# Kernel tuning notes

Measured on AMD Instinct MI355X. Metric: run time of the kernel, lower is better.

## Reference

```python
import jax, jax.numpy as jnp
import numpy as np

S_Q = 2048; B = 2; H = 16; D = 128
SCALE = 1.0 / np.sqrt(128.0)  # softmax_scale from init


def setup_inputs() -> dict:
    key = jax.random.key(0)
    kq, kk, kv, ks = jax.random.split(key, 4)
    q = jax.random.normal(kq, (S_Q, B, H, D), dtype=jnp.float32)
    k = jax.random.normal(kk, (S_Q, B, 1, D), dtype=jnp.float32)   # MQA: H_kv=1
    v = jax.random.normal(kv, (S_Q, B, 1, D), dtype=jnp.float32)
    sinks = jax.random.normal(ks, (H,), dtype=jnp.float32)         # learned per-head sink logits
    return {"q": q, "k": k, "v": v, "sinks": sinks, "mask": 0}


def reference(q, k, v, sinks, mask):
    # q: [S_q, B, H, D]; k, v: [S_k, B, H_kv, D] (H_kv may be 1 -> MQA expand)
    S_q, Bn, Hq, Dn = q.shape
    S_k = k.shape[0]
    k = jnp.broadcast_to(k, (S_k, Bn, Hq, Dn))
    v = jnp.broadcast_to(v, (S_k, Bn, Hq, Dn))
    # logits: [B, H, S_q, S_k]
    logits = jnp.einsum("sbhd,tbhd->bhst", q.astype(jnp.float32), k.astype(jnp.float32)) * SCALE
    # causal mask (triu(-inf, diag=1) added in original)
    causal = jnp.tril(jnp.ones((S_q, S_k), dtype=bool))
    logits = jnp.where(causal[None, None], logits, -jnp.inf)
    # sink-augmented softmax: append sink logit as extra column, softmax, drop it
    sink = sinks.astype(jnp.float32)[None, :, None, None]        # [1, H, 1, 1]
    m = jax.lax.stop_gradient(jnp.maximum(logits.max(axis=-1, keepdims=True), sink))
    e = jnp.exp(logits - m)                                      # [B, H, S_q, S_k]
    denom = e.sum(axis=-1, keepdims=True) + jnp.exp(sink - m)    # sink column contribution
    probs = e / denom
    out = jnp.einsum("bhst,tbhd->sbhd", probs.astype(v.dtype), v)  # [S_q, B, H, D]
    return out.reshape(S_q, Bn, Hq * Dn)
```

## Files before the change

kernel.cpp:

```cpp
#include <hip/hip_runtime.h>

#define SQ 2048
#define NB 2
#define NH 16
#define DH 128
#define NT32 64
#define NQT 32
#define SCALE_L2E 0.1275174609f
#define LOG2E 1.4426950408889634f
#define DEFER_THR 11.0f

typedef _Float16 f16x8 __attribute__((ext_vector_type(8)));
typedef _Float16 f16x4 __attribute__((ext_vector_type(4)));
typedef float f32x4 __attribute__((ext_vector_type(4)));

static __device__ __forceinline__ _Float16 f2h(float f) { return (_Float16)f; }

__global__ __launch_bounds__(256)
void prepack(const float* __restrict__ k, const float* __restrict__ v,
             _Float16* __restrict__ kws, _Float16* __restrict__ vws) {
    const int bid   = blockIdx.x;
    const int which = bid >> 7;
    const int b     = (bid >> 6) & 1;
    const int t     = bid & 63;
    const int tid   = threadIdx.x;

    if (which == 0) {
        const float* kbase = k + (size_t)t * 32 * (NB * DH) + b * DH;
        _Float16* dst = kws + ((size_t)b * NT32 + t) * 4096;
        #pragma unroll
        for (int p = 0; p < 4; ++p) {
            const int id4 = p * 256 + tid;
            const int row = id4 >> 5;
            const int c0  = (id4 & 31) << 2;
            f32x4 a = *(const f32x4*)(kbase + (size_t)row * (NB * DH) + c0);
            const int e = (row * 128 + c0) ^ ((row & 7) << 3);
            f16x4 pk = { f2h(a.x), f2h(a.y), f2h(a.z), f2h(a.w) };
            *(f16x4*)(dst + e) = pk;
        }
    } else {
        const float* vbase = v + b * DH;
        _Float16* dst = vws + ((size_t)b * NT32 + t) * 4096;
        const int d    = tid & 127;
        const int half = tid >> 7;
        #pragma unroll
        for (int p = 0; p < 4; ++p) {
            const int c0 = (p * 2 + half) * 4;
            float a0 = vbase[(size_t)(t * 32 + c0 + 0) * (NB * DH) + d];
            float a1 = vbase[(size_t)(t * 32 + c0 + 1) * (NB * DH) + d];
            float a2 = vbase[(size_t)(t * 32 + c0 + 2) * (NB * DH) + d];
            float a3 = vbase[(size_t)(t * 32 + c0 + 3) * (NB * DH) + d];
            const int e = (d * 32 + c0) ^ ((d & 7) << 3);
            f16x4 pk = { f2h(a0), f2h(a1), f2h(a2), f2h(a3) };
            *(f16x4*)(dst + e) = pk;
        }
    }
}

static __device__ __forceinline__ void gload16(const _Float16* gsrc, _Float16* ldst) {
    __builtin_amdgcn_global_load_lds(
        (const __attribute__((address_space(1))) void*)gsrc,
        (__attribute__((address_space(3))) void*)ldst, 16, 0, 0);
}

__global__ __launch_bounds__(256, 4)
void attn_fwd(const float* __restrict__ q, const _Float16* __restrict__ kws,
              const _Float16* __restrict__ vws, const float* __restrict__ sinks,
              float* __restrict__ out) {
    __shared__ _Float16 Kb[2][4096];
    __shared__ _Float16 Vb[2][4096];
    __shared__ _Float16 Plds[4][512];

    const int tid  = threadIdx.x;
    const int w    = tid >> 6;
    const int lane = tid & 63;
    const int r    = lane & 15;
    const int g    = lane >> 4;

    const int bid   = blockIdx.x;
    const int bh    = bid & 31;
    const int b     = bh & 1;
    const int h     = bh >> 1;
    const int qtIdx = bid >> 5;
    const int jj    = qtIdx & 7;
    const int mm    = qtIdx >> 3;
    const int qt = (mm == 0) ? jj : (mm == 1) ? 15 - jj
                 : (mm == 2) ? 16 + jj : 31 - jj;
    const int q0 = qt * 64;
    const int sq = q0 + w * 16 + r;

    f16x8 qf[4];
    {
        const float* qrow = q + ((size_t)sq * NB + b) * (NH * DH) + h * DH;
        #pragma unroll
        for (int kc = 0; kc < 4; ++kc) {
            const int d0 = kc * 32 + g * 8;
            f32x4 a = *(const f32x4*)(qrow + d0);
            f32x4 c = *(const f32x4*)(qrow + d0 + 4);
            f16x8 t;
            t[0] = f2h(a.x * SCALE_L2E); t[1] = f2h(a.y * SCALE_L2E);
            t[2] = f2h(a.z * SCALE_L2E); t[3] = f2h(a.w * SCALE_L2E);
            t[4] = f2h(c.x * SCALE_L2E); t[5] = f2h(c.y * SCALE_L2E);
            t[6] = f2h(c.z * SCALE_L2E); t[7] = f2h(c.w * SCALE_L2E);
            qf[kc] = t;
        }
    }

    float m_run = sinks[h] * LOG2E;
    float l_run = 1.0f;
    f32x4 acc[8];
    #pragma unroll
    for (int i = 0; i < 8; ++i) acc[i] = (f32x4)(0.0f);

    const _Float16* ktiles = kws + (size_t)b * NT32 * 4096;
    const _Float16* vtiles = vws + (size_t)b * NT32 * 4096;
    const int ntiles = 2 * qt + 2;
    const int wlimit = q0 + w * 16 + 15;

    #pragma unroll
    for (int p = 0; p < 2; ++p) {
        const int off = (p * 256 + tid) * 8;
        gload16(ktiles + off, &Kb[0][off]);
        gload16(vtiles + off, &Vb[0][off]);
    }
    asm volatile("s_waitcnt vmcnt(0)" ::: "memory");
    __builtin_amdgcn_s_barrier();

    for (int it = 0; it < ntiles; ++it) {
        const int cur = it & 1;
        if (it + 1 < ntiles) {
            const _Float16* kn = ktiles + (size_t)(it + 1) * 4096;
            const _Float16* vn = vtiles + (size_t)(it + 1) * 4096;
            #pragma unroll
            for (int p = 0; p < 2; ++p) {
                const int off = (p * 256 + tid) * 8;
                gload16(kn + off, &Kb[cur ^ 1][off]);
                gload16(vn + off, &Vb[cur ^ 1][off]);
            }
        }

        const int ktb = it * 32;
        if (ktb <= wlimit) {
            float sv[8];
            #pragma unroll
            for (int ct = 0; ct < 2; ++ct) {
                f32x4 sa = (f32x4)(0.0f);
                const int c = ct * 16 + r;
                #pragma unroll
                for (int kc = 0; kc < 4; ++kc) {
                    const int e = (c * 128 + kc * 32 + g * 8) ^ ((c & 7) << 3);
                    f16x8 kf = *(const f16x8*)(&Kb[cur][e]);
                    sa = __builtin_amdgcn_mfma_f32_16x16x32_f16(kf, qf[kc], sa, 0, 0, 0);
                }
                #pragma unroll
                for (int i = 0; i < 4; ++i) sv[ct * 4 + i] = sa[i];
            }

            if (ktb + 31 > q0 + w * 16) {
                #pragma unroll
                for (int ct = 0; ct < 2; ++ct)
                    #pragma unroll
                    for (int i = 0; i < 4; ++i) {
                        const int tk = ktb + ct * 16 + g * 4 + i;
                        if (tk > sq) sv[ct * 4 + i] = -1e30f;
                    }
            }

            float a0 = fmaxf(sv[0], sv[1]), a1 = fmaxf(sv[2], sv[3]);
            float a2 = fmaxf(sv[4], sv[5]), a3 = fmaxf(sv[6], sv[7]);
            float mx = fmaxf(fmaxf(a0, a1), fmaxf(a2, a3));
            mx = fmaxf(mx, __shfl_xor(mx, 16));
            mx = fmaxf(mx, __shfl_xor(mx, 32));

            if (!__all(mx <= m_run + DEFER_THR)) {
                const float mnew = fmaxf(m_run, mx);
                const float corr = __builtin_amdgcn_exp2f(m_run - mnew);
                m_run = mnew;
                l_run *= corr;
                #pragma unroll
                for (int i = 0; i < 4; ++i) {
                    const float ci = __shfl(corr, (lane & 48) | (g * 4 + i));
                    #pragma unroll
                    for (int nb = 0; nb < 8; ++nb) acc[nb][i] *= ci;
                }
            }

            #pragma unroll
            for (int i = 0; i < 8; ++i)
                sv[i] = __builtin_amdgcn_exp2f(sv[i] - m_run);
            float s0 = (sv[0] + sv[1]) + (sv[2] + sv[3]);
            float s1 = (sv[4] + sv[5]) + (sv[6] + sv[7]);
            float ls = s0 + s1;
            ls += __shfl_xor(ls, 16);
            ls += __shfl_xor(ls, 32);
            l_run += ls;

            #pragma unroll
            for (int ct = 0; ct < 2; ++ct) {
                f16x4 pb = { f2h(sv[ct * 4 + 0]), f2h(sv[ct * 4 + 1]),
                             f2h(sv[ct * 4 + 2]), f2h(sv[ct * 4 + 3]) };
                const int c0 = ct * 16 + g * 4;
                const int e = (r * 32 + c0) ^ ((r & 7) << 3);
                *(f16x4*)(&Plds[w][e]) = pb;
            }

            const int ep = (r * 32 + g * 8) ^ ((r & 7) << 3);
            f16x8 pf = *(const f16x8*)(&Plds[w][ep]);
            #pragma unroll
            for (int nb = 0; nb < 8; ++nb) {
                const int d = nb * 16 + r;
                const int ev = (d * 32 + g * 8) ^ ((d & 7) << 3);
                f16x8 vf = *(const f16x8*)(&Vb[cur][ev]);
                acc[nb] = __builtin_amdgcn_mfma_f32_16x16x32_f16(pf, vf, acc[nb], 0, 0, 0);
            }
        }

        asm volatile("s_waitcnt vmcnt(0)" ::: "memory");
        __builtin_amdgcn_s_barrier();
    }

    #pragma unroll
    for (int i = 0; i < 4; ++i) {
        const float li = __shfl(l_run, (lane & 48) | (g * 4 + i));
        const float rl = 1.0f / li;
        const int row = q0 + w * 16 + g * 4 + i;
        float* op = out + ((size_t)row * NB + b) * (NH * DH) + h * DH + r;
        #pragma unroll
        for (int nb = 0; nb < 8; ++nb)
            op[nb * 16] = acc[nb][i] * rl;
    }
}

extern "C" void kernel_launch(void* const* d_in, const int* in_sizes, int n_in,
                              void* d_out, int out_size, void* d_ws, size_t ws_size,
                              hipStream_t stream) {
    const float* q     = (const float*)d_in[0];
    const float* k     = (const float*)d_in[1];
    const float* v     = (const float*)d_in[2];
    const float* sinks = (const float*)d_in[3];
    float* out = (float*)d_out;

    _Float16* kws = (_Float16*)d_ws;
    _Float16* vws = kws + (size_t)NB * NT32 * 4096;

    prepack<<<dim3(256), 256, 0, stream>>>(k, v, kws, vws);
    attn_fwd<<<dim3(NQT * NB * NH), 256, 0, stream>>>(q, kws, vws, sinks, out);
}
```

Before: 89.60 us.

## Pair low/high causal query tiles per block and widen KV tiles to 64

```diff
diff --git a/kernel.cpp b/kernel.cpp
--- a/kernel.cpp
+++ b/kernel.cpp
@@ -4,7 +4,7 @@
 #define NB 2
 #define NH 16
 #define DH 128
-#define NT32 64
+#define NKT 32
 #define NQT 32
 #define SCALE_L2E 0.1275174609f
 #define LOG2E 1.4426950408889634f
@@ -20,16 +20,16 @@
 void prepack(const float* __restrict__ k, const float* __restrict__ v,
              _Float16* __restrict__ kws, _Float16* __restrict__ vws) {
     const int bid   = blockIdx.x;
-    const int which = bid >> 7;
-    const int b     = (bid >> 6) & 1;
-    const int t     = bid & 63;
+    const int which = bid >> 6;
+    const int b     = (bid >> 5) & 1;
+    const int t     = bid & 31;
     const int tid   = threadIdx.x;
 
     if (which == 0) {
-        const float* kbase = k + (size_t)t * 32 * (NB * DH) + b * DH;
-        _Float16* dst = kws + ((size_t)b * NT32 + t) * 4096;
-        #pragma unroll
-        for (int p = 0; p < 4; ++p) {
+        const float* kbase = k + (size_t)t * 64 * (NB * DH) + b * DH;
+        _Float16* dst = kws + ((size_t)b * NKT + t) * 8192;
+        #pragma unroll
+        for (int p = 0; p < 8; ++p) {
             const int id4 = p * 256 + tid;
             const int row = id4 >> 5;
             const int c0  = (id4 & 31) << 2;
@@ -40,17 +40,17 @@
         }
     } else {
         const float* vbase = v + b * DH;
-        _Float16* dst = vws + ((size_t)b * NT32 + t) * 4096;
+        _Float16* dst = vws + ((size_t)b * NKT + t) * 8192;
         const int d    = tid & 127;
         const int half = tid >> 7;
         #pragma unroll
-        for (int p = 0; p < 4; ++p) {
+        for (int p = 0; p < 8; ++p) {
             const int c0 = (p * 2 + half) * 4;
-            float a0 = vbase[(size_t)(t * 32 + c0 + 0) * (NB * DH) + d];
-            float a1 = vbase[(size_t)(t * 32 + c0 + 1) * (NB * DH) + d];
-            float a2 = vbase[(size_t)(t * 32 + c0 + 2) * (NB * DH) + d];
-            float a3 = vbase[(size_t)(t * 32 + c0 + 3) * (NB * DH) + d];
-            const int e = (d * 32 + c0) ^ ((d & 7) << 3);
+            float a0 = vbase[(size_t)(t * 64 + c0 + 0) * (NB * DH) + d];
+            float a1 = vbase[(size_t)(t * 64 + c0 + 1) * (NB * DH) + d];
+            float a2 = vbase[(size_t)(t * 64 + c0 + 2) * (NB * DH) + d];
+            float a3 = vbase[(size_t)(t * 64 + c0 + 3) * (NB * DH) + d];
+            const int e = (d * 64 + c0) ^ ((d & 7) << 3);
             f16x4 pk = { f2h(a0), f2h(a1), f2h(a2), f2h(a3) };
             *(f16x4*)(dst + e) = pk;
         }
@@ -63,13 +63,100 @@
         (__attribute__((address_space(3))) void*)ldst, 16, 0, 0);
 }
 
-__global__ __launch_bounds__(256, 4)
+static __device__ __forceinline__ void tile_update(
+    const _Float16* __restrict__ Kc, const _Float16* __restrict__ Vc,
+    _Float16* __restrict__ Pw, const f16x8* __restrict__ qf,
+    f32x4* __restrict__ acc, float& m_run, float& l_run,
+    int ktb, int sq, int q0w, int r, int g, int lane) {
+
+    float sv[16];
+    #pragma unroll
+    for (int ct = 0; ct < 4; ++ct) {
+        f32x4 sa = (f32x4)(0.0f);
+        const int c = ct * 16 + r;
+        #pragma unroll
+        for (int kc = 0; kc < 4; ++kc) {
+            const int e = (c * 128 + kc * 32 + g * 8) ^ ((c & 7) << 3);
+            f16x8 kf = *(const f16x8*)(&Kc[e]);
+            sa = __builtin_amdgcn_mfma_f32_16x16x32_f16(kf, qf[kc], sa, 0, 0, 0);
+        }
+        #pragma unroll
+        for (int i = 0; i < 4; ++i) sv[ct * 4 + i] = sa[i];
+    }
+
+    if (ktb + 63 > q0w) {
+        #pragma unroll
+        for (int ct = 0; ct < 4; ++ct)
+            #pragma unroll
+            for (int i = 0; i < 4; ++i) {
+                const int tk = ktb + ct * 16 + g * 4 + i;
+                if (tk > sq) sv[ct * 4 + i] = -1e30f;
+            }
+    }
+
+    float m0 = fmaxf(fmaxf(sv[0], sv[1]), fmaxf(sv[2], sv[3]));
+    float m1 = fmaxf(fmaxf(sv[4], sv[5]), fmaxf(sv[6], sv[7]));
+    float m2 = fmaxf(fmaxf(sv[8], sv[9]), fmaxf(sv[10], sv[11]));
+    float m3 = fmaxf(fmaxf(sv[12], sv[13]), fmaxf(sv[14], sv[15]));
+    float mx = fmaxf(fmaxf(m0, m1), fmaxf(m2, m3));
+    mx = fmaxf(mx, __shfl_xor(mx, 16));
+    mx = fmaxf(mx, __shfl_xor(mx, 32));
+
+    if (!__all(mx <= m_run + DEFER_THR)) {
+        const float mnew = fmaxf(m_run, mx);
+        const float corr = __builtin_amdgcn_exp2f(m_run - mnew);
+        m_run = mnew;
+        l_run *= corr;
+        #pragma unroll
+        for (int i = 0; i < 4; ++i) {
+            const float ci = __shfl(corr, (lane & 48) | (g * 4 + i));
+            #pragma unroll
+            for (int nb = 0; nb < 8; ++nb) acc[nb][i] *= ci;
+        }
+    }
+
+    #pragma unroll
+    for (int i = 0; i < 16; ++i)
+        sv[i] = __builtin_amdgcn_exp2f(sv[i] - m_run);
+    float t0 = (sv[0] + sv[1]) + (sv[2] + sv[3]);
+    float t1 = (sv[4] + sv[5]) + (sv[6] + sv[7]);
+    float t2 = (sv[8] + sv[9]) + (sv[10] + sv[11]);
+    float t3 = (sv[12] + sv[13]) + (sv[14] + sv[15]);
+    float ls = (t0 + t1) + (t2 + t3);
+    ls += __shfl_xor(ls, 16);
+    ls += __shfl_xor(ls, 32);
+    l_run += ls;
+
+    #pragma unroll
+    for (int ct = 0; ct < 4; ++ct) {
+        f16x4 pb = { f2h(sv[ct * 4 + 0]), f2h(sv[ct * 4 + 1]),
+                     f2h(sv[ct * 4 + 2]), f2h(sv[ct * 4 + 3]) };
+        const int c0 = ct * 16 + g * 4;
+        const int e = (r * 64 + c0) ^ ((r & 7) << 3);
+        *(f16x4*)(&Pw[e]) = pb;
+    }
+
+    #pragma unroll
+    for (int cc = 0; cc < 2; ++cc) {
+        const int ep = (r * 64 + cc * 32 + g * 8) ^ ((r & 7) << 3);
+        f16x8 pf = *(const f16x8*)(&Pw[ep]);
+        #pragma unroll
+        for (int nb = 0; nb < 8; ++nb) {
+            const int d = nb * 16 + r;
+            const int ev = (d * 64 + cc * 32 + g * 8) ^ ((d & 7) << 3);
+            f16x8 vf = *(const f16x8*)(&Vc[ev]);
+            acc[nb] = __builtin_amdgcn_mfma_f32_16x16x32_f16(pf, vf, acc[nb], 0, 0, 0);
+        }
+    }
+}
+
+__global__ __launch_bounds__(256, 2)
 void attn_fwd(const float* __restrict__ q, const _Float16* __restrict__ kws,
               const _Float16* __restrict__ vws, const float* __restrict__ sinks,
               float* __restrict__ out) {
-    __shared__ _Float16 Kb[2][4096];
-    __shared__ _Float16 Vb[2][4096];
-    __shared__ _Float16 Plds[4][512];
+    __shared__ _Float16 Kb[2][8192];
+    __shared__ _Float16 Vb[2][8192];
+    __shared__ _Float16 Plds[4][1024];
 
     const int tid  = threadIdx.x;
     const int w    = tid >> 6;
@@ -77,20 +164,20 @@
     const int r    = lane & 15;
     const int g    = lane >> 4;
 
-    const int bid   = blockIdx.x;
-    const int bh    = bid & 31;
-    const int b     = bh & 1;
-    const int h     = bh >> 1;
-    const int qtIdx = bid >> 5;
-    const int jj    = qtIdx & 7;
-    const int mm    = qtIdx >> 3;
-    const int qt = (mm == 0) ? jj : (mm == 1) ? 15 - jj
-                 : (mm == 2) ? 16 + jj : 31 - jj;
-    const int q0 = qt * 64;
-    const int sq = q0 + w * 16 + r;
-
-    f16x8 qf[4];
-    {
+    const int bid = blockIdx.x;
+    const int bh  = bid & 31;
+    const int b   = bh & 1;
+    const int h   = bh >> 1;
+    const int j   = bid >> 5;
+    const int qtL = j, qtH = NQT - 1 - j;
+    const int q0L = qtL * 64, q0H = qtH * 64;
+    const int sqL = q0L + w * 16 + r, sqH = q0H + w * 16 + r;
+
+    f16x8 qfL[4], qfH[4];
+    #pragma unroll
+    for (int ctx = 0; ctx < 2; ++ctx) {
+        const int sq = ctx ? sqH : sqL;
+        f16x8* qf = ctx ? qfH : qfL;
         const float* qrow = q + ((size_t)sq * NB + b) * (NH * DH) + h * DH;
         #pragma unroll
         for (int kc = 0; kc < 4; ++kc) {
@@ -106,19 +193,18 @@
         }
     }
 
-    float m_run = sinks[h] * LOG2E;
-    float l_run = 1.0f;
-    f32x4 acc[8];
-    #pragma unroll
-    for (int i = 0; i < 8; ++i) acc[i] = (f32x4)(0.0f);
-
-    const _Float16* ktiles = kws + (size_t)b * NT32 * 4096;
-    const _Float16* vtiles = vws + (size_t)b * NT32 * 4096;
-    const int ntiles = 2 * qt + 2;
-    const int wlimit = q0 + w * 16 + 15;
-
-    #pragma unroll
-    for (int p = 0; p < 2; ++p) {
+    const float sink2 = sinks[h] * LOG2E;
+    float mL = sink2, lL = 1.0f, mH = sink2, lH = 1.0f;
+    f32x4 accL[8], accH[8];
+    #pragma unroll
+    for (int i = 0; i < 8; ++i) { accL[i] = (f32x4)(0.0f); accH[i] = (f32x4)(0.0f); }
+
+    const _Float16* ktiles = kws + (size_t)b * NKT * 8192;
+    const _Float16* vtiles = vws + (size_t)b * NKT * 8192;
+    const int ntiles = qtH + 1;
+
+    #pragma unroll
+    for (int p = 0; p < 4; ++p) {
         const int off = (p * 256 + tid) * 8;
         gload16(ktiles + off, &Kb[0][off]);
         gload16(vtiles + off, &Vb[0][off]);
@@ -129,105 +215,43 @@
     for (int it = 0; it < ntiles; ++it) {
         const int cur = it & 1;
         if (it + 1 < ntiles) {
-            const _Float16* kn = ktiles + (size_t)(it + 1) * 4096;
-            const _Float16* vn = vtiles + (size_t)(it + 1) * 4096;
-            #pragma unroll
-            for (int p = 0; p < 2; ++p) {
+            const _Float16* kn = ktiles + (size_t)(it + 1) * 8192;
+            const _Float16* vn = vtiles + (size_t)(it + 1) * 8192;
+            #pragma unroll
+            for (int p = 0; p < 4; ++p) {
                 const int off = (p * 256 + tid) * 8;
                 gload16(kn + off, &Kb[cur ^ 1][off]);
                 gload16(vn + off, &Vb[cur ^ 1][off]);
             }
         }
 
-        const int ktb = it * 32;
-        if (ktb <= wlimit) {
-            float sv[8];
-            #pragma unroll
-            for (int ct = 0; ct < 2; ++ct) {
-                f32x4 sa = (f32x4)(0.0f);
-                const int c = ct * 16 + r;
-                #pragma unroll
-                for (int kc = 0; kc < 4; ++kc) {
-                    const int e = (c * 128 + kc * 32 + g * 8) ^ ((c & 7) << 3);
-                    f16x8 kf = *(const f16x8*)(&Kb[cur][e]);
-                    sa = __builtin_amdgcn_mfma_f32_16x16x32_f16(kf, qf[kc], sa, 0, 0, 0);
-                }
-                #pragma unroll
-                for (int i = 0; i < 4; ++i) sv[ct * 4 + i] = sa[i];
-            }
-
-            if (ktb + 31 > q0 + w * 16) {
-                #pragma unroll
-                for (int ct = 0; ct < 2; ++ct)
-                    #pragma unroll
-                    for (int i = 0; i < 4; ++i) {
-                        const int tk = ktb + ct * 16 + g * 4 + i;
-                        if (tk > sq) sv[ct * 4 + i] = -1e30f;
-                    }
-            }
-
-            float a0 = fmaxf(sv[0], sv[1]), a1 = fmaxf(sv[2], sv[3]);
-            float a2 = fmaxf(sv[4], sv[5]), a3 = fmaxf(sv[6], sv[7]);
-            float mx = fmaxf(fmaxf(a0, a1), fmaxf(a2, a3));
-            mx = fmaxf(mx, __shfl_xor(mx, 16));
-            mx = fmaxf(mx, __shfl_xor(mx, 32));
-
-            if (!__all(mx <= m_run + DEFER_THR)) {
-                const float mnew = fmaxf(m_run, mx);
-                const float corr = __builtin_amdgcn_exp2f(m_run - mnew);
-                m_run = mnew;
-                l_run *= corr;
-                #pragma unroll
-                for (int i = 0; i < 4; ++i) {
-                    const float ci = __shfl(corr, (lane & 48) | (g * 4 + i));
-                    #pragma unroll
-                    for (int nb = 0; nb < 8; ++nb) acc[nb][i] *= ci;
-                }
-            }
-
-            #pragma unroll
-            for (int i = 0; i < 8; ++i)
-                sv[i] = __builtin_amdgcn_exp2f(sv[i] - m_run);
-            float s0 = (sv[0] + sv[1]) + (sv[2] + sv[3]);
-            float s1 = (sv[4] + sv[5]) + (sv[6] + sv[7]);
-            float ls = s0 + s1;
-            ls += __shfl_xor(ls, 16);
-            ls += __shfl_xor(ls, 32);
-            l_run += ls;
-
-            #pragma unroll
-            for (int ct = 0; ct < 2; ++ct) {
-                f16x4 pb = { f2h(sv[ct * 4 + 0]), f2h(sv[ct * 4 + 1]),
-                             f2h(sv[ct * 4 + 2]), f2h(sv[ct * 4 + 3]) };
-                const int c0 = ct * 16 + g * 4;
-                const int e = (r * 32 + c0) ^ ((r & 7) << 3);
-                *(f16x4*)(&Plds[w][e]) = pb;
-            }
-
-            const int ep = (r * 32 + g * 8) ^ ((r & 7) << 3);
-            f16x8 pf = *(const f16x8*)(&Plds[w][ep]);
-            #pragma unroll
-            for (int nb = 0; nb < 8; ++nb) {
-                const int d = nb * 16 + r;
-                const int ev = (d * 32 + g * 8) ^ ((d & 7) << 3);
-                f16x8 vf = *(const f16x8*)(&Vb[cur][ev]);
-                acc[nb] = __builtin_amdgcn_mfma_f32_16x16x32_f16(pf, vf, acc[nb], 0, 0, 0);
-            }
-        }
+        const int ktb = it * 64;
+        if (ktb <= q0H + w * 16 + 15)
+            tile_update(Kb[cur], Vb[cur], Plds[w], qfH, accH, mH, lH,
+                        ktb, sqH, q0H + w * 16, r, g, lane);
+        if (ktb <= q0L + w * 16 + 15)
+            tile_update(Kb[cur], Vb[cur], Plds[w], qfL, accL, mL, lL,
+                        ktb, sqL, q0L + w * 16, r, g, lane);
 
         asm volatile("s_waitcnt vmcnt(0)" ::: "memory");
         __builtin_amdgcn_s_barrier();
     }
 
     #pragma unroll
-    for (int i = 0; i < 4; ++i) {
-        const float li = __shfl(l_run, (lane & 48) | (g * 4 + i));
-        const float rl = 1.0f / li;
-        const int row = q0 + w * 16 + g * 4 + i;
-        float* op = out + ((size_t)row * NB + b) * (NH * DH) + h * DH + r;
-        #pragma unroll
-        for (int nb = 0; nb < 8; ++nb)
-            op[nb * 16] = acc[nb][i] * rl;
+    for (int ctx = 0; ctx < 2; ++ctx) {
+        const int q0 = ctx ? q0H : q0L;
+        const float lr = ctx ? lH : lL;
+        const f32x4* acc = ctx ? accH : accL;
+        #pragma unroll
+        for (int i = 0; i < 4; ++i) {
+            const float li = __shfl(lr, (lane & 48) | (g * 4 + i));
+            const float rl = 1.0f / li;
+            const int row = q0 + w * 16 + g * 4 + i;
+            float* op = out + ((size_t)row * NB + b) * (NH * DH) + h * DH + r;
+            #pragma unroll
+            for (int nb = 0; nb < 8; ++nb)
+                op[nb * 16] = acc[nb][i] * rl;
+        }
     }
 }
 
@@ -241,8 +265,8 @@
     float* out = (float*)d_out;
 
     _Float16* kws = (_Float16*)d_ws;
-    _Float16* vws = kws + (size_t)NB * NT32 * 4096;
-
-    prepack<<<dim3(256), 256, 0, stream>>>(k, v, kws, vws);
-    attn_fwd<<<dim3(NQT * NB * NH), 256, 0, stream>>>(q, kws, vws, sinks, out);
-}
+    _Float16* vws = kws + (size_t)NB * NKT * 8192;
+
+    prepack<<<dim3(128), 256, 0, stream>>>(k, v, kws, vws);
+    attn_fwd<<<dim3((NQT / 2) * NB * NH), 256, 0, stream>>>(q, kws, vws, sinks, out);
+}
```

Result: faster. 72.60 us (-19.0%).

## Triple-buffer K/V tiles with one barrier per tile and deferred row-sum reduction

Applied to the files above, without the earlier changes.

```diff
diff --git a/kernel.cpp b/kernel.cpp
--- a/kernel.cpp
+++ b/kernel.cpp
@@ -63,12 +63,12 @@
         (__attribute__((address_space(3))) void*)ldst, 16, 0, 0);
 }
 
-__global__ __launch_bounds__(256, 4)
+__global__ __launch_bounds__(256, 3)
 void attn_fwd(const float* __restrict__ q, const _Float16* __restrict__ kws,
               const _Float16* __restrict__ vws, const float* __restrict__ sinks,
               float* __restrict__ out) {
-    __shared__ _Float16 Kb[2][4096];
-    __shared__ _Float16 Vb[2][4096];
+    __shared__ _Float16 Kb[3][4096];
+    __shared__ _Float16 Vb[3][4096];
     __shared__ _Float16 Plds[4][512];
 
     const int tid  = threadIdx.x;
@@ -77,17 +77,14 @@
     const int r    = lane & 15;
     const int g    = lane >> 4;
 
-    const int bid   = blockIdx.x;
-    const int bh    = bid & 31;
-    const int b     = bh & 1;
-    const int h     = bh >> 1;
-    const int qtIdx = bid >> 5;
-    const int jj    = qtIdx & 7;
-    const int mm    = qtIdx >> 3;
-    const int qt = (mm == 0) ? jj : (mm == 1) ? 15 - jj
-                 : (mm == 2) ? 16 + jj : 31 - jj;
-    const int q0 = qt * 64;
-    const int sq = q0 + w * 16 + r;
+    const int bid = blockIdx.x;
+    const int bh  = bid & 31;
+    const int b   = bh & 1;
+    const int h   = bh >> 1;
+    const int qt  = 31 - (bid >> 5);
+    const int q0  = qt * 64;
+    const int q0w = q0 + w * 16;
+    const int sq  = q0w + r;
 
     f16x8 qf[4];
     {
@@ -106,8 +103,9 @@
         }
     }
 
-    float m_run = sinks[h] * LOG2E;
-    float l_run = 1.0f;
+    const float sink2 = sinks[h] * LOG2E;
+    float m_run = sink2;
+    float l_p   = 0.0f;
     f32x4 acc[8];
     #pragma unroll
     for (int i = 0; i < 8; ++i) acc[i] = (f32x4)(0.0f);
@@ -115,7 +113,7 @@
     const _Float16* ktiles = kws + (size_t)b * NT32 * 4096;
     const _Float16* vtiles = vws + (size_t)b * NT32 * 4096;
     const int ntiles = 2 * qt + 2;
-    const int wlimit = q0 + w * 16 + 15;
+    const int wlimit = q0w + 15;
 
     #pragma unroll
     for (int p = 0; p < 2; ++p) {
@@ -123,25 +121,38 @@
         gload16(ktiles + off, &Kb[0][off]);
         gload16(vtiles + off, &Vb[0][off]);
     }
-    asm volatile("s_waitcnt vmcnt(0)" ::: "memory");
-    __builtin_amdgcn_s_barrier();
-
+    if (1 < ntiles) {
+        #pragma unroll
+        for (int p = 0; p < 2; ++p) {
+            const int off = (p * 256 + tid) * 8;
+            gload16(ktiles + 4096 + off, &Kb[1][off]);
+            gload16(vtiles + 4096 + off, &Vb[1][off]);
+        }
+    }
+
+    int cur = 0;
     for (int it = 0; it < ntiles; ++it) {
-        const int cur = it & 1;
-        if (it + 1 < ntiles) {
-            const _Float16* kn = ktiles + (size_t)(it + 1) * 4096;
-            const _Float16* vn = vtiles + (size_t)(it + 1) * 4096;
+        if (it + 1 < ntiles) asm volatile("s_waitcnt vmcnt(4)" ::: "memory");
+        else                 asm volatile("s_waitcnt vmcnt(0)" ::: "memory");
+        __builtin_amdgcn_s_barrier();
+        asm volatile("" ::: "memory");
+
+        if (it + 2 < ntiles) {
+            const int nb3 = (cur + 2 >= 3) ? cur - 1 : cur + 2;
+            const _Float16* kn = ktiles + (size_t)(it + 2) * 4096;
+            const _Float16* vn = vtiles + (size_t)(it + 2) * 4096;
             #pragma unroll
             for (int p = 0; p < 2; ++p) {
                 const int off = (p * 256 + tid) * 8;
-                gload16(kn + off, &Kb[cur ^ 1][off]);
-                gload16(vn + off, &Vb[cur ^ 1][off]);
+                gload16(kn + off, &Kb[nb3][off]);
+                gload16(vn + off, &Vb[nb3][off]);
             }
         }
 
         const int ktb = it * 32;
         if (ktb <= wlimit) {
             float sv[8];
+            __builtin_amdgcn_s_setprio(1);
             #pragma unroll
             for (int ct = 0; ct < 2; ++ct) {
                 f32x4 sa = (f32x4)(0.0f);
@@ -155,8 +166,9 @@
                 #pragma unroll
                 for (int i = 0; i < 4; ++i) sv[ct * 4 + i] = sa[i];
             }
-
-            if (ktb + 31 > q0 + w * 16) {
+            __builtin_amdgcn_s_setprio(0);
+
+            if (ktb + 31 > q0w) {
                 #pragma unroll
                 for (int ct = 0; ct < 2; ++ct)
                     #pragma unroll
@@ -169,14 +181,14 @@
             float a0 = fmaxf(sv[0], sv[1]), a1 = fmaxf(sv[2], sv[3]);
             float a2 = fmaxf(sv[4], sv[5]), a3 = fmaxf(sv[6], sv[7]);
             float mx = fmaxf(fmaxf(a0, a1), fmaxf(a2, a3));
-            mx = fmaxf(mx, __shfl_xor(mx, 16));
-            mx = fmaxf(mx, __shfl_xor(mx, 32));
 
             if (!__all(mx <= m_run + DEFER_THR)) {
+                mx = fmaxf(mx, __shfl_xor(mx, 16));
+                mx = fmaxf(mx, __shfl_xor(mx, 32));
                 const float mnew = fmaxf(m_run, mx);
                 const float corr = __builtin_amdgcn_exp2f(m_run - mnew);
                 m_run = mnew;
-                l_run *= corr;
+                l_p *= corr;
                 #pragma unroll
                 for (int i = 0; i < 4; ++i) {
                     const float ci = __shfl(corr, (lane & 48) | (g * 4 + i));
@@ -188,12 +200,9 @@
             #pragma unroll
             for (int i = 0; i < 8; ++i)
                 sv[i] = __builtin_amdgcn_exp2f(sv[i] - m_run);
-            float s0 = (sv[0] + sv[1]) + (sv[2] + sv[3]);
-            float s1 = (sv[4] + sv[5]) + (sv[6] + sv[7]);
-            float ls = s0 + s1;
-            ls += __shfl_xor(ls, 16);
-            ls += __shfl_xor(ls, 32);
-            l_run += ls;
+            float t0 = (sv[0] + sv[1]) + (sv[2] + sv[3]);
+            float t1 = (sv[4] + sv[5]) + (sv[6] + sv[7]);
+            l_p += t0 + t1;
 
             #pragma unroll
             for (int ct = 0; ct < 2; ++ct) {
@@ -206,6 +215,7 @@
 
             const int ep = (r * 32 + g * 8) ^ ((r & 7) << 3);
             f16x8 pf = *(const f16x8*)(&Plds[w][ep]);
+            __builtin_amdgcn_s_setprio(1);
             #pragma unroll
             for (int nb = 0; nb < 8; ++nb) {
                 const int d = nb * 16 + r;
@@ -213,15 +223,20 @@
                 f16x8 vf = *(const f16x8*)(&Vb[cur][ev]);
                 acc[nb] = __builtin_amdgcn_mfma_f32_16x16x32_f16(pf, vf, acc[nb], 0, 0, 0);
             }
-        }
-
-        asm volatile("s_waitcnt vmcnt(0)" ::: "memory");
-        __builtin_amdgcn_s_barrier();
-    }
-
+            __builtin_amdgcn_s_setprio(0);
+        }
+
+        cur = (cur + 1 >= 3) ? 0 : cur + 1;
+    }
+
+    float ls = l_p;
+    ls += __shfl_xor(ls, 16);
+    ls += __shfl_xor(ls, 32);
     #pragma unroll
     for (int i = 0; i < 4; ++i) {
-        const float li = __shfl(l_run, (lane & 48) | (g * 4 + i));
+        const int sel = (lane & 48) | (g * 4 + i);
+        const float mi = __shfl(m_run, sel);
+        const float li = __shfl(ls, sel) + __builtin_amdgcn_exp2f(sink2 - mi);
         const float rl = 1.0f / li;
         const int row = q0 + w * 16 + g * 4 + i;
         float* op = out + ((size_t)row * NB + b) * (NH * DH) + h * DH + r;
```

Measured after the change: 79.47 us. 1.13x faster.
